# Performance work log

Measured on AMD Instinct MI355X. Metric: run time of the kernel, lower is better.

## Reference

```python
import jax, jax.numpy as jnp
import numpy as np

EMBED = 1024
HEADS = 16
HEAD_DIM = EMBED // HEADS
NEG = -1e20


def setup_inputs() -> dict:
    key = jax.random.key(0)
    ks = jax.random.split(key, 12)
    N, L = 2, 2048
    lim_h = 1.0 / np.sqrt(HEAD_DIM)
    lim_e = 1.0 / np.sqrt(EMBED)
    u = lambda k, shape, lim: jax.random.uniform(k, shape, jnp.float32, -lim, lim)
    return {
        "query": jax.random.normal(ks[0], (N, L, EMBED), jnp.float32),
        "key": jax.random.normal(ks[1], (N, L, EMBED), jnp.float32),
        "value": jax.random.normal(ks[2], (N, L, EMBED), jnp.float32),
        "mask": jax.random.randint(ks[3], (N, 1, L, L), 0, 2, jnp.int32),
        "Wq": u(ks[4], (HEAD_DIM, HEAD_DIM), lim_h),
        "bq": u(ks[5], (HEAD_DIM,), lim_h),
        "Wk": u(ks[6], (HEAD_DIM, HEAD_DIM), lim_h),
        "bk": u(ks[7], (HEAD_DIM,), lim_h),
        "Wv": u(ks[8], (HEAD_DIM, HEAD_DIM), lim_h),
        "bv": u(ks[9], (HEAD_DIM,), lim_h),
        "Wo": u(ks[10], (EMBED, EMBED), lim_e),
        "bo": u(ks[11], (EMBED,), lim_e),
    }


def reference(query, key, value, mask, Wq, bq, Wk, bk, Wv, bv, Wo, bo):
    N, Lq, _ = query.shape
    Lk = key.shape[1]
    # split heads: [N, L, H, D]
    q = query.reshape(N, Lq, HEADS, HEAD_DIM)
    k = key.reshape(N, Lk, HEADS, HEAD_DIM)
    v = value.reshape(N, Lk, HEADS, HEAD_DIM)
    # shared per-head linear projections (torch Linear: x @ W.T + b)
    q = jnp.einsum('nlhd,ed->nlhe', q, Wq) + bq
    k = jnp.einsum('nlhd,ed->nlhe', k, Wk) + bk
    v = jnp.einsum('nlhd,ed->nlhe', v, Wv) + bv
    # scores [N, H, Q, K]
    energy = jnp.einsum('nqhd,nkhd->nhqk', q, k)
    # NOTE: original masks BEFORE scaling, and scales by sqrt(embed_size)
    energy = jnp.where(mask == 0, NEG, energy)
    energy = energy / jnp.sqrt(jnp.float32(EMBED))
    attn = jax.nn.softmax(energy, axis=-1)
    out = jnp.einsum('nhqk,nkhd->nqhd', attn, v)
    out = out.reshape(N, Lq, EMBED)
    return out @ Wo.T + bo
```

## Files before the change

### kernel.cpp

```cpp
#include <hip/hip_runtime.h>

#define NBATCH 2
#define SEQ 2048
#define EMBED 1024
#define HEADS 16
#define HDIM 64

typedef _Float16 h16x8 __attribute__((ext_vector_type(8)));
typedef _Float16 h16x4 __attribute__((ext_vector_type(4)));
typedef float f32x4 __attribute__((ext_vector_type(4)));
typedef unsigned long long u64;

__device__ __forceinline__ h16x8 f8h(const float* p) {
    const float4 a = *(const float4*)p;
    const float4 b = *(const float4*)(p + 4);
    h16x8 r;
    r[0] = (_Float16)a.x; r[1] = (_Float16)a.y;
    r[2] = (_Float16)a.z; r[3] = (_Float16)a.w;
    r[4] = (_Float16)b.x; r[5] = (_Float16)b.y;
    r[6] = (_Float16)b.z; r[7] = (_Float16)b.w;
    return r;
}

__global__ __launch_bounds__(256) void maskpack(const int* __restrict__ m,
                                                u64* __restrict__ mb)
{
    const size_t i = (size_t)blockIdx.x * 256 + threadIdx.x;
    const u64 b = __ballot(m[i] != 0);
    if ((threadIdx.x & 63) == 0) mb[i >> 6] = b;
}

__global__ __launch_bounds__(256) void cvt16(const float* __restrict__ in,
                                             _Float16* __restrict__ out, int n)
{
    const int i = (blockIdx.x * 256 + threadIdx.x) * 4;
    if (i < n) {
        const float4 v = *(const float4*)(in + i);
        h16x4 o;
        o[0] = (_Float16)v.x; o[1] = (_Float16)v.y;
        o[2] = (_Float16)v.z; o[3] = (_Float16)v.w;
        *(h16x4*)(out + i) = o;
    }
}

__global__ __launch_bounds__(256) void proj_kernel(
    const float* __restrict__ x, const float* __restrict__ W,
    const float* __restrict__ bias, _Float16* __restrict__ out, int transpose)
{
    const int wv = threadIdx.x >> 6;
    const int lane = threadIdx.x & 63;
    const int lr = lane & 15, lg = lane >> 4;
    const int nh = blockIdx.y, n = nh >> 4, h = nh & 15;
    const int lbase = blockIdx.x * 64 + wv * 16;

    const float* xrow = x + ((size_t)(n * SEQ + lbase + lr)) * EMBED + h * HDIM;
    const h16x8 a0 = f8h(xrow + lg * 8);
    const h16x8 a1 = f8h(xrow + 32 + lg * 8);

#pragma unroll
    for (int eb = 0; eb < 4; ++eb) {
        const float* wrow = W + (eb * 16 + lr) * HDIM;
        const h16x8 b0 = f8h(wrow + lg * 8);
        const h16x8 b1 = f8h(wrow + 32 + lg * 8);
        f32x4 c = {0.f, 0.f, 0.f, 0.f};
        c = __builtin_amdgcn_mfma_f32_16x16x32_f16(a0, b0, c, 0, 0, 0);
        c = __builtin_amdgcn_mfma_f32_16x16x32_f16(a1, b1, c, 0, 0, 0);
        const int col = eb * 16 + lr;
        const float bv = bias[col];
        if (!transpose) {
#pragma unroll
            for (int r = 0; r < 4; ++r) {
                const int row = lbase + lg * 4 + r;
                out[((size_t)nh * SEQ + row) * HDIM + col] = (_Float16)(c[r] + bv);
            }
        } else {
#pragma unroll
            for (int r = 0; r < 4; ++r) {
                const int row = lbase + lg * 4 + r;
                out[((size_t)nh * HDIM + col) * SEQ + row] = (_Float16)(c[r] + bv);
            }
        }
    }
}

__global__ __launch_bounds__(256, 4) void attn_kernel(
    const float* __restrict__ xq, const float* __restrict__ Wq,
    const float* __restrict__ bq,
    const _Float16* __restrict__ Kp, const _Float16* __restrict__ Vt,
    const u64* __restrict__ mbits, _Float16* __restrict__ Xo)
{
    __shared__ __align__(16) _Float16 qlds[4][16 * 64];
    __shared__ __align__(16) _Float16 plds[4][16 * 64];
    const int wv = threadIdx.x >> 6;
    const int lane = threadIdx.x & 63;
    const int lr = lane & 15, lg = lane >> 4;

    const int bid = blockIdx.x;
    const int sbid = (bid & 7) * 128 + (bid >> 3);
    const int nh = sbid >> 5, qt = sbid & 31;
    const int n = nh >> 4, h = nh & 15;
    const int qbase = qt * 64 + wv * 16;

    _Float16* qb_ = qlds[wv];
    _Float16* pb_ = plds[wv];

    {
        const float* xrow = xq + ((size_t)(n * SEQ + qbase + lr)) * EMBED + h * HDIM;
        const h16x8 a0 = f8h(xrow + lg * 8);
        const h16x8 a1 = f8h(xrow + 32 + lg * 8);
#pragma unroll
        for (int eb = 0; eb < 4; ++eb) {
            const float* wrow = Wq + (eb * 16 + lr) * HDIM;
            const h16x8 b0 = f8h(wrow + lg * 8);
            const h16x8 b1 = f8h(wrow + 32 + lg * 8);
            f32x4 c = {0.f, 0.f, 0.f, 0.f};
            c = __builtin_amdgcn_mfma_f32_16x16x32_f16(a0, b0, c, 0, 0, 0);
            c = __builtin_amdgcn_mfma_f32_16x16x32_f16(a1, b1, c, 0, 0, 0);
            const int col = eb * 16 + lr;
            const float bv = bq[col];
#pragma unroll
            for (int r = 0; r < 4; ++r) {
                const int row = lg * 4 + r;
                qb_[(row * 64 + col) ^ ((row & 7) << 3)] = (_Float16)(c[r] + bv);
            }
        }
    }
    asm volatile("s_waitcnt lgkmcnt(0)" ::: "memory");
    __builtin_amdgcn_sched_barrier(0);
    const h16x8 aq0 = *(const h16x8*)(qb_ + ((lr * 64 + lg * 8) ^ ((lr & 7) << 3)));
    const h16x8 aq1 = *(const h16x8*)(qb_ + ((lr * 64 + 32 + lg * 8) ^ ((lr & 7) << 3)));

    const u64* mrow = mbits + (size_t)n * SEQ * (SEQ / 64);
    const _Float16* kbase = Kp + (size_t)nh * SEQ * HDIM;
    const _Float16* vbase = Vt + (size_t)nh * HDIM * SEQ;

    const float SCL   = 0.0450842200277801f;
    const float NEGS2 = -1e20f * 0.0450842200277801f;
    const float THR2  = 11.5415603f;

    float m_[4], lsl[4];
    f32x4 o_[4];
#pragma unroll
    for (int r = 0; r < 4; ++r) { m_[r] = -3.0e38f; lsl[r] = 0.f; }
#pragma unroll
    for (int db = 0; db < 4; ++db) o_[db] = (f32x4){0.f, 0.f, 0.f, 0.f};

    for (int kb = 0; kb < SEQ; kb += 64) {
        h16x8 vf0[4], vf1[4];
#pragma unroll
        for (int db = 0; db < 4; ++db) {
            const _Float16* vr = vbase + (size_t)(db * 16 + lr) * SEQ + kb;
            vf0[db] = *(const h16x8*)(vr + lg * 8);
            vf1[db] = *(const h16x8*)(vr + 32 + lg * 8);
        }
        u64 mw[4];
#pragma unroll
        for (int r = 0; r < 4; ++r)
            mw[r] = mrow[(size_t)(qbase + lg * 4 + r) * (SEQ / 64) + (kb >> 6)];

        f32x4 s[4];
#pragma unroll
        for (int sg = 0; sg < 4; ++sg) {
            const _Float16* kr = kbase + (size_t)(kb + sg * 16 + lr) * HDIM;
            f32x4 c = {0.f, 0.f, 0.f, 0.f};
            c = __builtin_amdgcn_mfma_f32_16x16x32_f16(aq0, *(const h16x8*)(kr + lg * 8), c, 0, 0, 0);
            c = __builtin_amdgcn_mfma_f32_16x16x32_f16(aq1, *(const h16x8*)(kr + 32 + lg * 8), c, 0, 0, 0);
            s[sg] = c;
        }

        float tml[4];
#pragma unroll
        for (int r = 0; r < 4; ++r) {
            float t = -3.0e38f;
#pragma unroll
            for (int sg = 0; sg < 4; ++sg) {
                const bool on = (mw[r] >> (sg * 16 + lr)) & 1ull;
                s[sg][r] = on ? s[sg][r] * SCL : NEGS2;
                t = fmaxf(t, s[sg][r]);
            }
            tml[r] = t;
        }

        const bool ok = (tml[0] <= m_[0] + THR2) & (tml[1] <= m_[1] + THR2) &
                        (tml[2] <= m_[2] + THR2) & (tml[3] <= m_[3] + THR2);
        if (!__all(ok)) {
            float tm[4];
#pragma unroll
            for (int r = 0; r < 4; ++r) tm[r] = tml[r];
#pragma unroll
            for (int off = 1; off < 16; off <<= 1)
#pragma unroll
                for (int r = 0; r < 4; ++r) tm[r] = fmaxf(tm[r], __shfl_xor(tm[r], off));
#pragma unroll
            for (int r = 0; r < 4; ++r) {
                const float mn = fmaxf(m_[r], tm[r]);
                const float sc = exp2f(m_[r] - mn);
                m_[r] = mn;
                lsl[r] *= sc;
#pragma unroll
                for (int db = 0; db < 4; ++db) o_[db][r] *= sc;
            }
        }

#pragma unroll
        for (int sg = 0; sg < 4; ++sg)
#pragma unroll
            for (int r = 0; r < 4; ++r) {
                const float p = exp2f(s[sg][r] - m_[r]);
                lsl[r] += p;
                const int row = lg * 4 + r;
                pb_[(row * 64 + sg * 16 + lr) ^ ((row & 7) << 3)] = (_Float16)p;
            }

        asm volatile("s_waitcnt lgkmcnt(0)" ::: "memory");
        __builtin_amdgcn_sched_barrier(0);
        const h16x8 pa0 = *(const h16x8*)(pb_ + ((lr * 64 + lg * 8) ^ ((lr & 7) << 3)));
        const h16x8 pa1 = *(const h16x8*)(pb_ + ((lr * 64 + 32 + lg * 8) ^ ((lr & 7) << 3)));

#pragma unroll
        for (int db = 0; db < 4; ++db) {
            o_[db] = __builtin_amdgcn_mfma_f32_16x16x32_f16(pa0, vf0[db], o_[db], 0, 0, 0);
            o_[db] = __builtin_amdgcn_mfma_f32_16x16x32_f16(pa1, vf1[db], o_[db], 0, 0, 0);
        }
    }

#pragma unroll
    for (int off = 1; off < 16; off <<= 1)
#pragma unroll
        for (int r = 0; r < 4; ++r) lsl[r] += __shfl_xor(lsl[r], off);
#pragma unroll
    for (int r = 0; r < 4; ++r) {
        const float inv = 1.0f / lsl[r];
        const int qr = qbase + lg * 4 + r;
        _Float16* orow = Xo + ((size_t)n * SEQ + qr) * EMBED + h * HDIM;
#pragma unroll
        for (int db = 0; db < 4; ++db)
            orow[db * 16 + lr] = (_Float16)(o_[db][r] * inv);
    }
}

__global__ __launch_bounds__(256, 4) void outproj_mfma(
    const _Float16* __restrict__ X, const _Float16* __restrict__ Wo16,
    const float* __restrict__ bo, float* __restrict__ out)
{
    const int wv = threadIdx.x >> 6;
    const int lane = threadIdx.x & 63;
    const int lr = lane & 15, lg = lane >> 4;
    const int rbase = blockIdx.y * 64 + wv * 16;
    const int cbase = blockIdx.x * 64;

    f32x4 acc[4];
#pragma unroll
    for (int cb = 0; cb < 4; ++cb) acc[cb] = (f32x4){0.f, 0.f, 0.f, 0.f};

    const _Float16* xrow = X + (size_t)(rbase + lr) * EMBED;
#pragma unroll 2
    for (int k0 = 0; k0 < EMBED; k0 += 32) {
        const h16x8 a = *(const h16x8*)(xrow + k0 + lg * 8);
#pragma unroll
        for (int cb = 0; cb < 4; ++cb) {
            const h16x8 b = *(const h16x8*)(Wo16 + (size_t)(cbase + cb * 16 + lr) * EMBED + k0 + lg * 8);
            acc[cb] = __builtin_amdgcn_mfma_f32_16x16x32_f16(a, b, acc[cb], 0, 0, 0);
        }
    }
#pragma unroll
    for (int cb = 0; cb < 4; ++cb) {
        const int col = cbase + cb * 16 + lr;
        const float bv = bo[col];
#pragma unroll
        for (int r = 0; r < 4; ++r) {
            const int row = rbase + lg * 4 + r;
            out[(size_t)row * EMBED + col] = acc[cb][r] + bv;
        }
    }
}

extern "C" void kernel_launch(void* const* d_in, const int* in_sizes, int n_in,
                              void* d_out, int out_size, void* d_ws, size_t ws_size,
                              hipStream_t stream)
{
    const float* q    = (const float*)d_in[0];
    const float* k    = (const float*)d_in[1];
    const float* v    = (const float*)d_in[2];
    const int*  mask  = (const int*)d_in[3];
    const float* Wq   = (const float*)d_in[4];
    const float* bq   = (const float*)d_in[5];
    const float* Wk   = (const float*)d_in[6];
    const float* bk   = (const float*)d_in[7];
    const float* Wv   = (const float*)d_in[8];
    const float* bv   = (const float*)d_in[9];
    const float* Wo   = (const float*)d_in[10];
    const float* bo   = (const float*)d_in[11];

    const size_t per = (size_t)NBATCH * HEADS * SEQ * HDIM;
    const size_t nmask = (size_t)NBATCH * SEQ * SEQ;
    u64*      mbits = (u64*)d_ws;
    _Float16* Kp    = (_Float16*)(mbits + nmask / 64);
    _Float16* Vt    = Kp + per;
    _Float16* Xh    = Vt + per;
    _Float16* Wo16  = Xh + per;

    maskpack<<<(int)(nmask / 256), 256, 0, stream>>>(mask, mbits);
    cvt16<<<EMBED * EMBED / 1024, 256, 0, stream>>>(Wo, Wo16, EMBED * EMBED);
    const dim3 pgrid(SEQ / 64, NBATCH * HEADS);
    proj_kernel<<<pgrid, 256, 0, stream>>>(k, Wk, bk, Kp, 0);
    proj_kernel<<<pgrid, 256, 0, stream>>>(v, Wv, bv, Vt, 1);
    attn_kernel<<<1024, 256, 0, stream>>>(q, Wq, bq, Kp, Vt, mbits, Xh);
    outproj_mfma<<<dim3(EMBED / 64, NBATCH * SEQ / 64), 256, 0, stream>>>(Xh, Wo16, bo, (float*)d_out);
}
```

Baseline: 478.9 us.

## Split attention over key range with combine pass; LDS-tiled wider out-projection

Attention work is split into two halves along the key sequence (flash-decoding style). Each half writes a normalized partial output plus its max and sum, and a new combine kernel merges the two halves with log-sum-exp weights. This doubles the block count to 2048 to improve occupancy and load balance, at the cost of extra partial-output traffic and one more launch. The output projection now stages Wo tiles in swizzled LDS and computes 128 columns per block to increase reuse. The split path only runs if the workspace is large enough.

Result: slower. 880.6 us (+83.9%).

```diff
diff --git a/kernel.cpp b/kernel.cpp
--- a/kernel.cpp
+++ b/kernel.cpp
@@ -83,11 +83,12 @@
     }
 }
 
-__global__ __launch_bounds__(256, 4) void attn_kernel(
+__global__ __launch_bounds__(256, 8) void attn_kernel(
     const float* __restrict__ xq, const float* __restrict__ Wq,
     const float* __restrict__ bq,
     const _Float16* __restrict__ Kp, const _Float16* __restrict__ Vt,
-    const u64* __restrict__ mbits, _Float16* __restrict__ Xo)
+    const u64* __restrict__ mbits, _Float16* __restrict__ Xo,
+    _Float16* __restrict__ pO, float2* __restrict__ pML, int nsplit)
 {
     __shared__ __align__(16) _Float16 qlds[4][16 * 64];
     __shared__ __align__(16) _Float16 plds[4][16 * 64];
@@ -96,10 +97,14 @@
     const int lr = lane & 15, lg = lane >> 4;
 
     const int bid = blockIdx.x;
-    const int sbid = (bid & 7) * 128 + (bid >> 3);
-    const int nh = sbid >> 5, qt = sbid & 31;
+    const int sbid = (bid & 7) * (128 * nsplit) + (bid >> 3);
+    const int half = sbid % nsplit;
+    const int qtnh = sbid / nsplit;
+    const int qt = qtnh & 31, nh = qtnh >> 5;
     const int n = nh >> 4, h = nh & 15;
     const int qbase = qt * 64 + wv * 16;
+    const int klen = SEQ / nsplit;
+    const int kbeg = half * klen;
 
     _Float16* qb_ = qlds[wv];
     _Float16* pb_ = plds[wv];
@@ -145,7 +150,7 @@
 #pragma unroll
     for (int db = 0; db < 4; ++db) o_[db] = (f32x4){0.f, 0.f, 0.f, 0.f};
 
-    for (int kb = 0; kb < SEQ; kb += 64) {
+    for (int kb = kbeg; kb < kbeg + klen; kb += 64) {
         h16x8 vf0[4], vf1[4];
 #pragma unroll
         for (int db = 0; db < 4; ++db) {
@@ -228,48 +233,103 @@
     for (int off = 1; off < 16; off <<= 1)
 #pragma unroll
         for (int r = 0; r < 4; ++r) lsl[r] += __shfl_xor(lsl[r], off);
-#pragma unroll
-    for (int r = 0; r < 4; ++r) {
-        const float inv = 1.0f / lsl[r];
-        const int qr = qbase + lg * 4 + r;
-        _Float16* orow = Xo + ((size_t)n * SEQ + qr) * EMBED + h * HDIM;
-#pragma unroll
-        for (int db = 0; db < 4; ++db)
-            orow[db * 16 + lr] = (_Float16)(o_[db][r] * inv);
-    }
-}
-
-__global__ __launch_bounds__(256, 4) void outproj_mfma(
+
+    if (nsplit == 1) {
+#pragma unroll
+        for (int r = 0; r < 4; ++r) {
+            const float inv = 1.0f / lsl[r];
+            const int qr = qbase + lg * 4 + r;
+            _Float16* orow = Xo + ((size_t)n * SEQ + qr) * EMBED + h * HDIM;
+#pragma unroll
+            for (int db = 0; db < 4; ++db)
+                orow[db * 16 + lr] = (_Float16)(o_[db][r] * inv);
+        }
+    } else {
+        const int pid = sbid;
+#pragma unroll
+        for (int r = 0; r < 4; ++r) {
+            const float inv = 1.0f / lsl[r];
+            const int row = wv * 16 + lg * 4 + r;
+            _Float16* prow = pO + ((size_t)pid * 64 + row) * 64;
+#pragma unroll
+            for (int db = 0; db < 4; ++db)
+                prow[db * 16 + lr] = (_Float16)(o_[db][r] * inv);
+            if (lr == 0) pML[(size_t)pid * 64 + row] = make_float2(m_[r], lsl[r]);
+        }
+    }
+}
+
+__global__ __launch_bounds__(256) void combine_kernel(
+    const _Float16* __restrict__ pO, const float2* __restrict__ pML,
+    _Float16* __restrict__ Xh)
+{
+    const int b = blockIdx.x;
+    const int nh = b >> 5, qt = b & 31;
+    const int n = nh >> 4, h = nh & 15;
+    const int row = threadIdx.x >> 2, dg = threadIdx.x & 3;
+    const int pid0 = b * 2, pid1 = pid0 + 1;
+
+    const float2 ml1 = pML[(size_t)pid0 * 64 + row];
+    const float2 ml2 = pML[(size_t)pid1 * 64 + row];
+    const float m = fmaxf(ml1.x, ml2.x);
+    const float w1 = ml1.y * exp2f(ml1.x - m);
+    const float w2 = ml2.y * exp2f(ml2.x - m);
+    const float inv = 1.0f / (w1 + w2);
+    const float a1 = w1 * inv, a2 = w2 * inv;
+
+    const _Float16* p1 = pO + ((size_t)pid0 * 64 + row) * 64 + dg * 16;
+    const _Float16* p2 = pO + ((size_t)pid1 * 64 + row) * 64 + dg * 16;
+    _Float16* xr = Xh + ((size_t)n * SEQ + qt * 64 + row) * EMBED + h * HDIM + dg * 16;
+#pragma unroll
+    for (int j = 0; j < 16; ++j)
+        xr[j] = (_Float16)(a1 * (float)p1[j] + a2 * (float)p2[j]);
+}
+
+__global__ __launch_bounds__(256, 2) void outproj_mfma(
     const _Float16* __restrict__ X, const _Float16* __restrict__ Wo16,
     const float* __restrict__ bo, float* __restrict__ out)
 {
+    __shared__ __align__(16) _Float16 Bs[128 * 64];
     const int wv = threadIdx.x >> 6;
     const int lane = threadIdx.x & 63;
     const int lr = lane & 15, lg = lane >> 4;
-    const int rbase = blockIdx.y * 64 + wv * 16;
-    const int cbase = blockIdx.x * 64;
-
-    f32x4 acc[4];
-#pragma unroll
-    for (int cb = 0; cb < 4; ++cb) acc[cb] = (f32x4){0.f, 0.f, 0.f, 0.f};
-
-    const _Float16* xrow = X + (size_t)(rbase + lr) * EMBED;
-#pragma unroll 2
-    for (int k0 = 0; k0 < EMBED; k0 += 32) {
-        const h16x8 a = *(const h16x8*)(xrow + k0 + lg * 8);
-#pragma unroll
-        for (int cb = 0; cb < 4; ++cb) {
-            const h16x8 b = *(const h16x8*)(Wo16 + (size_t)(cbase + cb * 16 + lr) * EMBED + k0 + lg * 8);
-            acc[cb] = __builtin_amdgcn_mfma_f32_16x16x32_f16(a, b, acc[cb], 0, 0, 0);
-        }
-    }
-#pragma unroll
-    for (int cb = 0; cb < 4; ++cb) {
+    const int rbase = blockIdx.y * 64;
+    const int cbase = blockIdx.x * 128;
+
+    f32x4 acc[8];
+#pragma unroll
+    for (int cb = 0; cb < 8; ++cb) acc[cb] = (f32x4){0.f, 0.f, 0.f, 0.f};
+
+    const _Float16* xrow = X + (size_t)(rbase + wv * 16 + lr) * EMBED;
+    const int sc_ = threadIdx.x >> 1, skk = (threadIdx.x & 1) * 32;
+    const _Float16* ssrc = Wo16 + (size_t)(cbase + sc_) * EMBED + skk;
+    _Float16* sdst = Bs + sc_ * 64;
+    const int ssw = (sc_ & 7) << 3;
+
+    for (int k0 = 0; k0 < EMBED; k0 += 64) {
+        __syncthreads();
+#pragma unroll
+        for (int j = 0; j < 4; ++j)
+            *(h16x8*)(sdst + ((skk + j * 8) ^ ssw)) = *(const h16x8*)(ssrc + k0 + j * 8);
+        __syncthreads();
+#pragma unroll
+        for (int kk2 = 0; kk2 < 2; ++kk2) {
+            const h16x8 a = *(const h16x8*)(xrow + k0 + kk2 * 32 + lg * 8);
+#pragma unroll
+            for (int cb = 0; cb < 8; ++cb) {
+                const int c = cb * 16 + lr;
+                const h16x8 b = *(const h16x8*)(Bs + c * 64 + ((kk2 * 32 + lg * 8) ^ ((c & 7) << 3)));
+                acc[cb] = __builtin_amdgcn_mfma_f32_16x16x32_f16(a, b, acc[cb], 0, 0, 0);
+            }
+        }
+    }
+#pragma unroll
+    for (int cb = 0; cb < 8; ++cb) {
         const int col = cbase + cb * 16 + lr;
         const float bv = bo[col];
 #pragma unroll
         for (int r = 0; r < 4; ++r) {
-            const int row = rbase + lg * 4 + r;
+            const int row = rbase + wv * 16 + lg * 4 + r;
             out[(size_t)row * EMBED + col] = acc[cb][r] + bv;
         }
     }
@@ -299,12 +359,18 @@
     _Float16* Vt    = Kp + per;
     _Float16* Xh    = Vt + per;
     _Float16* Wo16  = Xh + per;
+    _Float16* pO    = Wo16 + (size_t)EMBED * EMBED;
+    float2*   pML   = (float2*)(pO + (size_t)2048 * 64 * 64);
+    const size_t need = 46137344;
+    const int nsplit = (ws_size >= need) ? 2 : 1;
 
     maskpack<<<(int)(nmask / 256), 256, 0, stream>>>(mask, mbits);
     cvt16<<<EMBED * EMBED / 1024, 256, 0, stream>>>(Wo, Wo16, EMBED * EMBED);
     const dim3 pgrid(SEQ / 64, NBATCH * HEADS);
     proj_kernel<<<pgrid, 256, 0, stream>>>(k, Wk, bk, Kp, 0);
     proj_kernel<<<pgrid, 256, 0, stream>>>(v, Wv, bv, Vt, 1);
-    attn_kernel<<<1024, 256, 0, stream>>>(q, Wq, bq, Kp, Vt, mbits, Xh);
-    outproj_mfma<<<dim3(EMBED / 64, NBATCH * SEQ / 64), 256, 0, stream>>>(Xh, Wo16, bo, (float*)d_out);
-}
+    attn_kernel<<<1024 * nsplit, 256, 0, stream>>>(q, Wq, bq, Kp, Vt, mbits, Xh, pO, pML, nsplit);
+    if (nsplit == 2)
+        combine_kernel<<<1024, 256, 0, stream>>>(pO, pML, Xh);
+    outproj_mfma<<<dim3(EMBED / 128, NBATCH * SEQ / 64), 256, 0, stream>>>(Xh, Wo16, bo, (float*)d_out);
+}
```
